# Performance work log

Hardware: AMD Instinct MI355X
Metric: run time of the kernel (lower is better)

## Reference

```python
import jax, jax.numpy as jnp
import numpy as np

B, N, C, H = 64, 198, 768, 12
D = C // H  # head_dim = 64


def lsq_binary(x, alpha):
    """Elastic (LSQ-style) symmetric binarization with STE: out = alpha*sign(x/alpha)."""
    xs = x / alpha
    return alpha * (xs + jax.lax.stop_gradient(jnp.sign(xs) - xs))


def lsq_bin01(x, alpha):
    """Asymmetric binarization to levels {0, alpha} with STE (for post-softmax attention)."""
    xs = x / alpha
    qh = jnp.clip(jnp.round(xs), 0.0, 1.0)
    return alpha * (xs + jax.lax.stop_gradient(qh - xs))


def gsb(x, alphas, bin_fn):
    """Group-superposition binarization: sum of residual binarizations with per-group scales."""
    out = jnp.zeros_like(x)
    r = x
    for a in alphas:  # fixed small loop over 3 groups
        b = bin_fn(r, a)
        out = out + b
        r = r - b
    return out


def bwn(w):
    """Binary-weight-network weight fake-quant (layerwise scale = mean|w|) with STE."""
    q = jnp.mean(jnp.abs(w)) * jnp.sign(w)
    return w + jax.lax.stop_gradient(q - w)


def setup_inputs() -> dict:
    key = jax.random.key(0)
    ks = jax.random.split(key, 8)
    one = jnp.ones((), jnp.float32)
    return {
        "x": jax.random.normal(ks[0], (B, N, C), jnp.float32),
        "qkv_w": jax.random.normal(ks[1], (3 * C, C), jnp.float32) * 0.02,
        "proj_w": jax.random.normal(ks[2], (C, C), jnp.float32) * 0.02,
        "proj_b": jnp.zeros((C,), jnp.float32),
        "move_q_b": jax.random.normal(ks[3], (H, 1, D), jnp.float32) * 0.01,
        "move_k_b": jax.random.normal(ks[4], (H, 1, D), jnp.float32) * 0.01,
        "move_v_b": jax.random.normal(ks[5], (H, 1, D), jnp.float32) * 0.01,
        "move_att_b": jax.random.normal(ks[6], (H, N, N), jnp.float32) * 0.01,
        "clip_in_qkv": one, "clip_query": one, "clip_key": one,
        "clip_v1": one, "clip_v2": one * 0.5, "clip_v3": one * 0.25,
        "clip_a1": one, "clip_a2": one * 0.5, "clip_a3": one * 0.25,
        "clip_in_proj": one,
    }


def reference(x, qkv_w, proj_w, proj_b, move_q_b, move_k_b, move_v_b, move_att_b,
              clip_in_qkv, clip_query, clip_key, clip_v1, clip_v2, clip_v3,
              clip_a1, clip_a2, clip_a3, clip_in_proj):
    b, n, c = x.shape
    scale = D ** -0.5
    # quantized qkv projection (binary act, BWN weight)
    xq = lsq_binary(x, clip_in_qkv)
    qkv = jnp.einsum('bnc,oc->bno', xq, bwn(qkv_w))  # [B,N,3C]
    qkv = qkv.reshape(b, n, 3, H, D).transpose(2, 0, 3, 1, 4)  # [3,B,H,N,D]
    q, k, v = qkv[0], qkv[1], qkv[2]
    # learnable per-head bias shifts, then fake-quant
    q = lsq_binary(q + move_q_b, clip_query)
    k = lsq_binary(k + move_k_b, clip_key)
    v = gsb(v + move_v_b, (clip_v1, clip_v2, clip_v3), lsq_binary)
    attn = jax.nn.softmax(jnp.einsum('bhnd,bhmd->bhnm', q, k) * scale, axis=-1)
    attn = attn + move_att_b  # [H,N,N] broadcast over batch
    attn = gsb(attn, (clip_a1, clip_a2, clip_a3), lsq_bin01)
    out = jnp.einsum('bhnm,bhmd->bhnd', attn, v).transpose(0, 2, 1, 3).reshape(b, n, c)
    # quantized output projection
    outq = lsq_binary(out, clip_in_proj)
    return jnp.einsum('bnc,oc->bno', outq, bwn(proj_w)) + proj_b
```

## Files before the change

kernel.cpp:

```cpp
#include <hip/hip_runtime.h>
#include <hip/hip_bf16.h>

typedef __attribute__((ext_vector_type(8))) short short8;
typedef __attribute__((ext_vector_type(4))) float f32x4;
typedef __attribute__((ext_vector_type(4))) int int4v;
typedef __attribute__((ext_vector_type(8))) char char8v;
typedef __attribute__((ext_vector_type(4), aligned(4))) unsigned int uint4a;

static constexpr int B = 64, N = 198, C = 768, H = 12, D = 64;
static constexpr int M = B * N;
static constexpr int BH = B * H;
static constexpr int O3C = 3 * C;
static constexpr int NXB = 99;
static constexpr int TLD8 = 144;
static constexpr int AL8 = 272;
static constexpr int VNP = 256;

static constexpr size_t OFF_MEANS = 0;
static constexpr size_t OFF_TAB   = 256;
static constexpr size_t OFF_PARTA = 2048;
static constexpr size_t OFF_PARTP = 4096;
static constexpr size_t OFF_XS    = 8192;
static constexpr size_t SZ_XS     = (size_t)M * C;
static constexpr size_t OFF_WQS   = OFF_XS + SZ_XS;
static constexpr size_t SZ_WQS    = (size_t)O3C * C;
static constexpr size_t OFF_WPS   = OFF_WQS + SZ_WQS;
static constexpr size_t SZ_WPS    = (size_t)C * C;
static constexpr size_t OFF_Q     = OFF_WPS + SZ_WPS;
static constexpr size_t SZ_QK8    = (size_t)BH * N * D;
static constexpr size_t OFF_K     = OFF_Q + SZ_QK8;
static constexpr size_t OFF_VT    = OFF_K + SZ_QK8;
static constexpr size_t SZ_VT8    = (size_t)BH * D * VNP;
static constexpr size_t OFF_OS    = OFF_VT + SZ_VT8;

#define GLOAD_LDS16(g, l)                                                  \
  __builtin_amdgcn_global_load_lds(                                        \
      (const __attribute__((address_space(1))) void*)(g),                  \
      (__attribute__((address_space(3))) void*)(l), 16, 0, 0)

__global__ void reduce_abs2_kernel(const float* __restrict__ qw, int nq,
                                   const float* __restrict__ pw, int np,
                                   double* __restrict__ partA, double* __restrict__ partP) {
  __shared__ double sm[256];
  const float* src;
  int n, b;
  double* dst;
  if (blockIdx.x < 256) { src = qw; n = nq; dst = partA; b = blockIdx.x; }
  else                  { src = pw; n = np; dst = partP; b = blockIdx.x - 256; }
  double s = 0.0;
  for (int i = b * 256 + threadIdx.x; i < n; i += 256 * 256)
    s += (double)fabsf(src[i]);
  sm[threadIdx.x] = s;
  __syncthreads();
  for (int off = 128; off > 0; off >>= 1) {
    if (threadIdx.x < (unsigned)off) sm[threadIdx.x] += sm[threadIdx.x + off];
    __syncthreads();
  }
  if (threadIdx.x == 0) dst[b] = sm[0];
}

__global__ void finalize_kernel(const double* __restrict__ pA, const double* __restrict__ pP,
                                double* __restrict__ means, double* __restrict__ tab,
                                const float* cq, const float* ck) {
  __shared__ double sm[256];
  int t = threadIdx.x;
  sm[t] = pA[t];
  __syncthreads();
  for (int off = 128; off > 0; off >>= 1) { if (t < off) sm[t] += sm[t + off]; __syncthreads(); }
  if (t == 0) means[0] = sm[0] / (double)((size_t)O3C * C);
  __syncthreads();
  sm[t] = pP[t];
  __syncthreads();
  for (int off = 128; off > 0; off >>= 1) { if (t < off) sm[t] += sm[t + off]; __syncthreads(); }
  if (t == 0) means[1] = sm[0] / (double)((size_t)C * C);
  double delta = (double)cq[0] * (double)ck[0] * 0.125;
  if (t < 129) tab[t] = exp((double)(t - 128) * delta);
  if (t < 16) tab[129 + t] = exp((double)t * delta);
}

__global__ void sign8_all_kernel(const float* __restrict__ x, signed char* __restrict__ Xs,
                                 const float* __restrict__ qw, signed char* __restrict__ Wq,
                                 const float* __restrict__ pw, signed char* __restrict__ Wp,
                                 int nx8, int nq8, int np8, const float* alpha) {
  float a = alpha[0];
  signed char posx = (a > 0.0f) ? 1 : ((a < 0.0f) ? -1 : 0);
  int total = nx8 + nq8 + np8;
  int stride = 256 * gridDim.x;
  for (int i = blockIdx.x * 256 + threadIdx.x; i < total; i += stride) {
    const float* src;
    signed char* dst;
    int j;
    signed char pos;
    if (i < nx8) { src = x; dst = Xs; j = i; pos = posx; }
    else if (i < nx8 + nq8) { src = qw; dst = Wq; j = i - nx8; pos = 1; }
    else { src = pw; dst = Wp; j = i - nx8 - nq8; pos = 1; }
    signed char neg = (signed char)(-pos);
    const float4* xp = (const float4*)(src + (size_t)j * 8);
    float4 u = xp[0], v = xp[1];
    float vals[8] = {u.x, u.y, u.z, u.w, v.x, v.y, v.z, v.w};
    char8v s;
#pragma unroll
    for (int k = 0; k < 8; ++k)
      s[k] = vals[k] > 0.0f ? pos : (vals[k] < 0.0f ? neg : (signed char)0);
    *(char8v*)(dst + (size_t)j * 8) = s;
  }
}

static __device__ inline bool xcd_decode(int lin, int nyb, int& x, int& y) {
  int k = lin & 7;
  int q = lin >> 3;
  int xi = q / nyb;
  y = q - xi * nyb;
  x = xi * 8 + k;
  return x < NXB;
}

static __device__ inline void stage_i8(const signed char* __restrict__ A,
                                       const signed char* __restrict__ Bmat,
                                       int i0, int o0, int k0,
                                       char* AsB, char* BsB) {
  int tid = threadIdx.x;
  int lane = tid & 63, w = tid >> 6;
#pragma unroll
  for (int c = 0; c < 2; ++c) {
    int ccb = w * 64 + c * 256;
    int cc = ccb + lane;
    int row = cc >> 2, cwl = cc & 3;
    int sc16 = (cwl ^ ((row >> 1) & 3)) * 16;
    GLOAD_LDS16(&A[(size_t)(i0 + row) * C + k0 + sc16], AsB + (size_t)ccb * 16);
    GLOAD_LDS16(&Bmat[(size_t)(o0 + row) * C + k0 + sc16], BsB + (size_t)ccb * 16);
  }
}

static __device__ inline void compute_i8(const signed char (*As)[64],
                                         const signed char (*Bs)[64],
                                         int4v acc[4][4]) {
  int lane = threadIdx.x & 63, w = threadIdx.x >> 6, wr = w >> 1, wc = w & 1;
  int g = lane >> 4;
  int4v af[4], bf[4];
#pragma unroll
  for (int m = 0; m < 4; ++m) {
    int row = wr * 64 + m * 16 + (lane & 15);
    af[m] = *(const int4v*)&As[row][((g ^ ((row >> 1) & 3))) * 16];
  }
#pragma unroll
  for (int n2 = 0; n2 < 4; ++n2) {
    int row = wc * 64 + n2 * 16 + (lane & 15);
    bf[n2] = *(const int4v*)&Bs[row][((g ^ ((row >> 1) & 3))) * 16];
  }
  __builtin_amdgcn_s_setprio(1);
#pragma unroll
  for (int m = 0; m < 4; ++m)
#pragma unroll
    for (int n2 = 0; n2 < 4; ++n2)
      acc[m][n2] = __builtin_amdgcn_mfma_i32_16x16x64_i8(af[m], bf[n2], acc[m][n2], 0, 0, 0);
  __builtin_amdgcn_s_setprio(0);
}

static __device__ inline void gemm_dbuf_i8(const signed char* __restrict__ A,
                                           const signed char* __restrict__ Bmat,
                                           int i0, int o0, char* smem, int4v acc[4][4]) {
  stage_i8(A, Bmat, i0, o0, 0, smem, smem + 8192);
  asm volatile("s_waitcnt vmcnt(0)" ::: "memory");
  __builtin_amdgcn_sched_barrier(0);
  __builtin_amdgcn_s_barrier();
#pragma unroll
  for (int t = 0; t < 12; ++t) {
    const int cu = t & 1;
    if (t < 11)
      stage_i8(A, Bmat, i0, o0, (t + 1) * 64,
               smem + (cu ^ 1) * 16384, smem + (cu ^ 1) * 16384 + 8192);
    compute_i8((const signed char(*)[64])(smem + cu * 16384),
               (const signed char(*)[64])(smem + cu * 16384 + 8192), acc);
    if (t < 11) {
      asm volatile("s_waitcnt vmcnt(0)" ::: "memory");
      __builtin_amdgcn_sched_barrier(0);
      __builtin_amdgcn_s_barrier();
    }
  }
}

__global__ __launch_bounds__(256) void gemm1_kernel(
    const signed char* __restrict__ Xs, const signed char* __restrict__ Wqs,
    const double* __restrict__ means,
    const float* cin, const float* cq, const float* ck,
    const float* cv1, const float* cv2, const float* cv3,
    const float* __restrict__ movq, const float* __restrict__ movk, const float* __restrict__ movv,
    signed char* __restrict__ Qs8, signed char* __restrict__ Ks8, signed char* __restrict__ Vt8) {
  int bx, by;
  if (!xcd_decode(blockIdx.x, O3C / 128, bx, by)) return;
  __shared__ __align__(16) char smem[32768];
  signed char* tile8 = (signed char*)smem;
  int4v acc[4][4] = {};
  int i0 = bx * 128, o0 = by * 128;
  gemm_dbuf_i8(Xs, Wqs, i0, o0, smem, acc);
  int tid = threadIdx.x;
  int lane = tid & 63, w = tid >> 6, wr = w >> 1, wc = w & 1;
  double cw_ = (double)cin[0] * means[0];
  float dq = cq[0], dk = ck[0];
  signed char sq8 = dq > 0.0f ? 1 : (dq < 0.0f ? -1 : 0);
  signed char sk8 = dk > 0.0f ? 1 : (dk < 0.0f ? -1 : 0);
  double aa1 = fabs((double)cv1[0]), aa2 = fabs((double)cv2[0]), aa3 = fabs((double)cv3[0]);
  int t = o0 / C;
  int rem0 = o0 - t * C;
  signed char sg8 = t == 0 ? sq8 : sk8;
  const float* mov = t == 0 ? movq : (t == 1 ? movk : movv);
  __syncthreads();
#pragma unroll
  for (int m = 0; m < 4; ++m)
#pragma unroll
    for (int n2 = 0; n2 < 4; ++n2)
#pragma unroll
      for (int r = 0; r < 4; ++r) {
        int rowL = wr * 64 + m * 16 + (lane >> 4) * 4 + r;
        int colL = wc * 64 + n2 * 16 + (lane & 15);
        int rem = rem0 + colL;
        int h = rem >> 6, d = rem & 63;
        double g = (double)acc[m][n2][r] * cw_;
        if (t < 2) {
          double v = g + (double)mov[h * D + d];
          tile8[rowL * TLD8 + colL] = v > 0.0 ? sg8 : (v < 0.0 ? (signed char)(-sg8) : (signed char)0);
        } else {
          double rr = g + (double)mov[h * D + d];
          double b1 = rr > 0.0 ? aa1 : (rr < 0.0 ? -aa1 : 0.0);
          rr -= b1;
          double b2 = rr > 0.0 ? aa2 : (rr < 0.0 ? -aa2 : 0.0);
          rr -= b2;
          double b3 = rr > 0.0 ? aa3 : (rr < 0.0 ? -aa3 : 0.0);
          tile8[colL * TLD8 + rowL] = (signed char)(int)rint(4.0 * (b1 + b2 + b3));
        }
      }
  __syncthreads();
  if (t < 2) {
    signed char* dst = t == 0 ? Qs8 : Ks8;
#pragma unroll
    for (int it = 0; it < 4; ++it) {
      int c = tid + it * 256;
      int rowL = c >> 3, cch = c & 7;
      int gr = i0 + rowL;
      int b = gr / N, nn = gr - b * N;
      int rem = rem0 + cch * 16;
      int h = rem >> 6, d = rem & 63;
      *(uint4a*)&dst[((size_t)(b * H + h) * N + nn) * 64 + d] =
          *(const uint4a*)&tile8[rowL * TLD8 + cch * 16];
    }
  } else {
#pragma unroll
    for (int it = 0; it < 4; ++it) {
      int c = tid + it * 256;
      int colL = c >> 3, tch = c & 7;
      int rem = rem0 + colL;
      int h = rem >> 6, d = rem & 63;
      int gr0 = i0 + tch * 16;
      int b0 = gr0 / N, nn0 = gr0 - b0 * N;
      if (nn0 + 16 <= N) {
        *(uint4a*)&Vt8[((size_t)(b0 * H + h) * 64 + d) * VNP + nn0] =
            *(const uint4a*)&tile8[colL * TLD8 + tch * 16];
      } else {
#pragma unroll
        for (int j = 0; j < 16; ++j) {
          int gr = gr0 + j;
          int b = gr / N, nn = gr - b * N;
          Vt8[((size_t)(b * H + h) * 64 + d) * VNP + nn] = tile8[colL * TLD8 + tch * 16 + j];
        }
      }
    }
  }
}

__global__ __launch_bounds__(256) void attn_kernel(
    const signed char* __restrict__ Qs8, const signed char* __restrict__ Ks8,
    const signed char* __restrict__ Vt8, const double* __restrict__ tab,
    const float* __restrict__ movatt,
    const float* ca1p, const float* ca2p, const float* ca3p, const float* cipp,
    signed char* __restrict__ Os) {
  __shared__ double Tl1[9];
  __shared__ double Tl2[16];
  __shared__ signed char Al8[4][16 * AL8];
  int i = blockIdx.x;
  int xcd = i & 7;
  int q = i >> 3;
  int rt = q % 13;
  int grp = q / 13;
  int tid = threadIdx.x;
  int w = tid >> 6, lane = tid & 63;
  int bh = (grp * 4 + w) * 8 + xcd;
  int b = bh / H, h = bh - b * H;
  int g = lane >> 4, q16 = lane & 15;
  if (tid < 9) Tl1[tid] = tab[16 * tid];
  if (tid >= 32 && tid < 48) Tl2[tid - 32] = tab[129 + (tid - 32)];
  for (int ii = lane; ii < 192; ii += 64) {
    int row = ii / 12, cd = ii - row * 12;
    *(int*)&Al8[w][row * AL8 + 208 + cd * 4] = 0;
  }
  __syncthreads();
  double ca1 = (double)ca1p[0], ca2 = (double)ca2p[0], ca3 = (double)ca3p[0];
  double t1 = 0.5 * ca1, t2 = 0.5 * ca2, t3 = 0.5 * ca3;
  int q1 = (int)rint(4.0 * ca1), q2 = (int)rint(4.0 * ca2), q3 = (int)rint(4.0 * ca3);
  float cip = cipp[0];
  signed char cp = cip > 0.0f ? 1 : (cip < 0.0f ? -1 : 0);

  int4v qf = {};
  int qrow = rt * 16 + q16;
  if (qrow < N) qf = *(const int4v*)&Qs8[((size_t)bh * N + qrow) * 64 + g * 16];
  int4v sacc[13] = {};
#pragma unroll
  for (int ct = 0; ct < 13; ++ct) {
    int krow = ct * 16 + q16;
    int4v kf = {};
    if (krow < N) kf = *(const int4v*)&Ks8[((size_t)bh * N + krow) * 64 + g * 16];
    sacc[ct] = __builtin_amdgcn_mfma_i32_16x16x64_i8(qf, kf, sacc[ct], 0, 0, 0);
  }
#pragma unroll
  for (int r = 0; r < 4; ++r) {
    int rowg = rt * 16 + g * 4 + r;
    int rowc = rowg < N ? rowg : N - 1;
    const float* mrow = movatt + ((size_t)h * N + rowc) * N;
    int mx = -1000000;
#pragma unroll
    for (int ct = 0; ct < 13; ++ct) {
      int colc = ct * 16 + q16;
      if (colc < N) mx = max(mx, sacc[ct][r]);
    }
    mx = max(mx, __shfl_xor(mx, 1));
    mx = max(mx, __shfl_xor(mx, 2));
    mx = max(mx, __shfl_xor(mx, 4));
    mx = max(mx, __shfl_xor(mx, 8));
    double ev[13];
    double ssum = 0.0;
#pragma unroll
    for (int ct = 0; ct < 13; ++ct) {
      int colc = ct * 16 + q16;
      int idx = sacc[ct][r] - mx + 128;
      idx = idx > 128 ? 128 : idx;
      double e = (colc < N) ? Tl1[idx >> 4] * Tl2[idx & 15] : 0.0;
      ev[ct] = e;
      ssum += e;
    }
    ssum += __shfl_xor(ssum, 1);
    ssum += __shfl_xor(ssum, 2);
    ssum += __shfl_xor(ssum, 4);
    ssum += __shfl_xor(ssum, 8);
    double rec = 1.0 / ssum;
#pragma unroll
    for (int ct = 0; ct < 13; ++ct) {
      int colc = ct * 16 + q16;
      int colb = colc < N ? colc : N - 1;
      double at = ev[ct] * rec + (double)mrow[colb];
      int p4 = 0;
      double rr = at;
      if (rr > t1) { p4 += q1; rr -= ca1; }
      if (rr > t2) { p4 += q2; rr -= ca2; }
      if (rr > t3) { p4 += q3; }
      Al8[w][(g * 4 + r) * AL8 + colc] = (signed char)((colc < N) ? p4 : 0);
    }
  }
  int4v oacc[4] = {};
#pragma unroll
  for (int kt = 0; kt < 4; ++kt) {
    int4v af = *(const int4v*)&Al8[w][q16 * AL8 + kt * 64 + g * 16];
#pragma unroll
    for (int dt = 0; dt < 4; ++dt) {
      int4v bv = *(const int4v*)&Vt8[((size_t)bh * 64 + dt * 16 + q16) * VNP + kt * 64 + g * 16];
      oacc[dt] = __builtin_amdgcn_mfma_i32_16x16x64_i8(af, bv, oacc[dt], 0, 0, 0);
    }
  }
#pragma unroll
  for (int dt = 0; dt < 4; ++dt)
#pragma unroll
    for (int r = 0; r < 4; ++r) {
      int rowg = rt * 16 + g * 4 + r;
      if (rowg < N) {
        int d = dt * 16 + q16;
        int s = oacc[dt][r];
        Os[((size_t)(b * N + rowg)) * C + h * D + d] =
            s > 0 ? cp : (s < 0 ? (signed char)(-cp) : (signed char)0);
      }
    }
}

__global__ __launch_bounds__(256) void gemm2_kernel(
    const signed char* __restrict__ Os, const signed char* __restrict__ Wps,
    const double* __restrict__ means, const float* cip, const float* __restrict__ proj_b,
    float* __restrict__ out) {
  int bx, by;
  if (!xcd_decode(blockIdx.x, C / 128, bx, by)) return;
  __shared__ __align__(16) char smem[32768];
  int4v acc[4][4] = {};
  int i0 = bx * 128, o0 = by * 128;
  gemm_dbuf_i8(Os, Wps, i0, o0, smem, acc);
  int lane = threadIdx.x & 63, w = threadIdx.x >> 6, wr = w >> 1, wc = w & 1;
  double cw_ = (double)cip[0] * means[1];
#pragma unroll
  for (int m = 0; m < 4; ++m)
#pragma unroll
    for (int n2 = 0; n2 < 4; ++n2)
#pragma unroll
      for (int r = 0; r < 4; ++r) {
        int row = i0 + wr * 64 + m * 16 + (lane >> 4) * 4 + r;
        int col = o0 + wc * 64 + n2 * 16 + (lane & 15);
        double v = (double)acc[m][n2][r] * cw_ + (double)proj_b[col];
        out[(size_t)row * C + col] = (float)v;
      }
}

extern "C" void kernel_launch(void* const* d_in, const int* in_sizes, int n_in,
                              void* d_out, int out_size, void* d_ws, size_t ws_size,
                              hipStream_t stream) {
  const float* x      = (const float*)d_in[0];
  const float* qkv_w  = (const float*)d_in[1];
  const float* proj_w = (const float*)d_in[2];
  const float* proj_b = (const float*)d_in[3];
  const float* movq   = (const float*)d_in[4];
  const float* movk   = (const float*)d_in[5];
  const float* movv   = (const float*)d_in[6];
  const float* movatt = (const float*)d_in[7];
  const float* c_inq  = (const float*)d_in[8];
  const float* c_q    = (const float*)d_in[9];
  const float* c_k    = (const float*)d_in[10];
  const float* c_v1   = (const float*)d_in[11];
  const float* c_v2   = (const float*)d_in[12];
  const float* c_v3   = (const float*)d_in[13];
  const float* c_a1   = (const float*)d_in[14];
  const float* c_a2   = (const float*)d_in[15];
  const float* c_a3   = (const float*)d_in[16];
  const float* c_inp  = (const float*)d_in[17];

  char* ws = (char*)d_ws;
  double* means = (double*)(ws + OFF_MEANS);
  double* tab   = (double*)(ws + OFF_TAB);
  double* partA = (double*)(ws + OFF_PARTA);
  double* partP = (double*)(ws + OFF_PARTP);
  signed char* Xs  = (signed char*)(ws + OFF_XS);
  signed char* Wqs = (signed char*)(ws + OFF_WQS);
  signed char* Wps = (signed char*)(ws + OFF_WPS);
  signed char* Qs8 = (signed char*)(ws + OFF_Q);
  signed char* Ks8 = (signed char*)(ws + OFF_K);
  signed char* Vt8 = (signed char*)(ws + OFF_VT);
  signed char* Os  = (signed char*)(ws + OFF_OS);

  reduce_abs2_kernel<<<512, 256, 0, stream>>>(qkv_w, O3C * C, proj_w, C * C, partA, partP);
  finalize_kernel<<<1, 256, 0, stream>>>(partA, partP, means, tab, c_q, c_k);
  sign8_all_kernel<<<2048, 256, 0, stream>>>(x, Xs, qkv_w, Wqs, proj_w, Wps,
                                             M * C / 8, O3C * C / 8, C * C / 8, c_inq);
  gemm1_kernel<<<104 * (O3C / 128), 256, 0, stream>>>(
      Xs, Wqs, means, c_inq, c_q, c_k, c_v1, c_v2, c_v3, movq, movk, movv, Qs8, Ks8, Vt8);
  attn_kernel<<<8 * 13 * (BH / 32), 256, 0, stream>>>(Qs8, Ks8, Vt8, tab, movatt, c_a1, c_a2, c_a3, c_inp, Os);
  gemm2_kernel<<<104 * (C / 128), 256, 0, stream>>>(
      Os, Wps, means, c_inp, proj_b, (float*)d_out);
}
```

Before: 161.4 us.

## Pre-tile int8 operands into MFMA fragment layout and load GEMM fragments directly from global

The sign kernel now writes X, qkv weights and proj weights in a 16-row x 64-byte fragment-tiled layout. The attention kernel writes its output in the same layout, so each MFMA operand becomes one contiguous 16-byte-per-lane load. Both GEMMs drop the LDS double-buffered staging and barriers and read fragments straight from global memory into registers. Tiles change to 64x256, with each wave owning 64 output columns. This removes LDS traffic and sync overhead, but loses LDS reuse across waves and has no explicit prefetch, so global load latency may be exposed.

```diff
diff --git a/kernel.cpp b/kernel.cpp
--- a/kernel.cpp
+++ b/kernel.cpp
@@ -11,10 +11,14 @@
 static constexpr int M = B * N;
 static constexpr int BH = B * H;
 static constexpr int O3C = 3 * C;
-static constexpr int NXB = 99;
-static constexpr int TLD8 = 144;
+static constexpr int KC = 48;
+static constexpr int NXT = 198;
+static constexpr int NXTP = 200;
 static constexpr int AL8 = 272;
 static constexpr int VNP = 256;
+static constexpr int TLQ = 272;
+static constexpr int TLV = 80;
+
 
 static constexpr size_t OFF_MEANS = 0;
 static constexpr size_t OFF_TAB   = 256;
@@ -33,11 +37,6 @@
 static constexpr size_t SZ_VT8    = (size_t)BH * D * VNP;
 static constexpr size_t OFF_OS    = OFF_VT + SZ_VT8;
 
-#define GLOAD_LDS16(g, l)                                                  \
-  __builtin_amdgcn_global_load_lds(                                        \
-      (const __attribute__((address_space(1))) void*)(g),                  \
-      (__attribute__((address_space(3))) void*)(l), 16, 0, 0)
-
 __global__ void reduce_abs2_kernel(const float* __restrict__ qw, int nq,
                                    const float* __restrict__ pw, int np,
                                    double* __restrict__ partA, double* __restrict__ partP) {
@@ -78,105 +77,66 @@
   if (t < 16) tab[129 + t] = exp((double)t * delta);
 }
 
-__global__ void sign8_all_kernel(const float* __restrict__ x, signed char* __restrict__ Xs,
-                                 const float* __restrict__ qw, signed char* __restrict__ Wq,
-                                 const float* __restrict__ pw, signed char* __restrict__ Wp,
-                                 int nx8, int nq8, int np8, const float* alpha) {
+__global__ void sign8_tiled_kernel(const float* __restrict__ x, signed char* __restrict__ Xs,
+                                   const float* __restrict__ qw, signed char* __restrict__ Wq,
+                                   const float* __restrict__ pw, signed char* __restrict__ Wp,
+                                   int ux, int uq, int up, const float* alpha) {
   float a = alpha[0];
   signed char posx = (a > 0.0f) ? 1 : ((a < 0.0f) ? -1 : 0);
-  int total = nx8 + nq8 + np8;
+  int total = ux + uq + up;
   int stride = 256 * gridDim.x;
-  for (int i = blockIdx.x * 256 + threadIdx.x; i < total; i += stride) {
+  for (int u = blockIdx.x * 256 + threadIdx.x; u < total; u += stride) {
     const float* src;
     signed char* dst;
     int j;
     signed char pos;
-    if (i < nx8) { src = x; dst = Xs; j = i; pos = posx; }
-    else if (i < nx8 + nq8) { src = qw; dst = Wq; j = i - nx8; pos = 1; }
-    else { src = pw; dst = Wp; j = i - nx8 - nq8; pos = 1; }
+    if (u < ux) { src = x; dst = Xs; j = u; pos = posx; }
+    else if (u < ux + uq) { src = qw; dst = Wq; j = u - ux; pos = 1; }
+    else { src = pw; dst = Wp; j = u - ux - uq; pos = 1; }
     signed char neg = (signed char)(-pos);
-    const float4* xp = (const float4*)(src + (size_t)j * 8);
-    float4 u = xp[0], v = xp[1];
-    float vals[8] = {u.x, u.y, u.z, u.w, v.x, v.y, v.z, v.w};
-    char8v s;
-#pragma unroll
-    for (int k = 0; k < 8; ++k)
-      s[k] = vals[k] > 0.0f ? pos : (vals[k] < 0.0f ? neg : (signed char)0);
-    *(char8v*)(dst + (size_t)j * 8) = s;
-  }
-}
-
-static __device__ inline bool xcd_decode(int lin, int nyb, int& x, int& y) {
+    int row = j / KC, kc = j - row * KC;
+    const float4* xp = (const float4*)(src + (size_t)row * C + kc * 16);
+    signed char out16[16];
+#pragma unroll
+    for (int q4 = 0; q4 < 4; ++q4) {
+      float4 v = xp[q4];
+      float vv[4] = {v.x, v.y, v.z, v.w};
+#pragma unroll
+      for (int k = 0; k < 4; ++k)
+        out16[q4 * 4 + k] = vv[k] > 0.0f ? pos : (vv[k] < 0.0f ? neg : (signed char)0);
+    }
+    size_t off = (((size_t)(row >> 4) * KC + kc) * 16 + (row & 15)) * 16;
+    *(uint4a*)(dst + off) = *(const uint4a*)out16;
+  }
+}
+
+static __device__ inline bool xcd_decode(int lin, int nyb, int limit, int& x, int& y) {
   int k = lin & 7;
   int q = lin >> 3;
   int xi = q / nyb;
   y = q - xi * nyb;
   x = xi * 8 + k;
-  return x < NXB;
-}
-
-static __device__ inline void stage_i8(const signed char* __restrict__ A,
-                                       const signed char* __restrict__ Bmat,
-                                       int i0, int o0, int k0,
-                                       char* AsB, char* BsB) {
-  int tid = threadIdx.x;
-  int lane = tid & 63, w = tid >> 6;
-#pragma unroll
-  for (int c = 0; c < 2; ++c) {
-    int ccb = w * 64 + c * 256;
-    int cc = ccb + lane;
-    int row = cc >> 2, cwl = cc & 3;
-    int sc16 = (cwl ^ ((row >> 1) & 3)) * 16;
-    GLOAD_LDS16(&A[(size_t)(i0 + row) * C + k0 + sc16], AsB + (size_t)ccb * 16);
-    GLOAD_LDS16(&Bmat[(size_t)(o0 + row) * C + k0 + sc16], BsB + (size_t)ccb * 16);
-  }
-}
-
-static __device__ inline void compute_i8(const signed char (*As)[64],
-                                         const signed char (*Bs)[64],
-                                         int4v acc[4][4]) {
-  int lane = threadIdx.x & 63, w = threadIdx.x >> 6, wr = w >> 1, wc = w & 1;
-  int g = lane >> 4;
-  int4v af[4], bf[4];
-#pragma unroll
-  for (int m = 0; m < 4; ++m) {
-    int row = wr * 64 + m * 16 + (lane & 15);
-    af[m] = *(const int4v*)&As[row][((g ^ ((row >> 1) & 3))) * 16];
-  }
-#pragma unroll
-  for (int n2 = 0; n2 < 4; ++n2) {
-    int row = wc * 64 + n2 * 16 + (lane & 15);
-    bf[n2] = *(const int4v*)&Bs[row][((g ^ ((row >> 1) & 3))) * 16];
-  }
-  __builtin_amdgcn_s_setprio(1);
-#pragma unroll
-  for (int m = 0; m < 4; ++m)
+  return x < limit;
+}
+
+static __device__ inline void gemm_reg_i8(const signed char* __restrict__ At,
+                                          const signed char* __restrict__ Bt,
+                                          int x4, int nt0, int4v acc[4][4]) {
+  int lane = threadIdx.x & 63;
+#pragma unroll
+  for (int t = 0; t < 12; ++t) {
+    int4v af[4], bf[4];
+#pragma unroll
+    for (int m = 0; m < 4; ++m)
+      af[m] = *(const int4v*)&At[((size_t)(x4 + m) * KC + t * 4) * 256 + lane * 16];
 #pragma unroll
     for (int n2 = 0; n2 < 4; ++n2)
-      acc[m][n2] = __builtin_amdgcn_mfma_i32_16x16x64_i8(af[m], bf[n2], acc[m][n2], 0, 0, 0);
-  __builtin_amdgcn_s_setprio(0);
-}
-
-static __device__ inline void gemm_dbuf_i8(const signed char* __restrict__ A,
-                                           const signed char* __restrict__ Bmat,
-                                           int i0, int o0, char* smem, int4v acc[4][4]) {
-  stage_i8(A, Bmat, i0, o0, 0, smem, smem + 8192);
-  asm volatile("s_waitcnt vmcnt(0)" ::: "memory");
-  __builtin_amdgcn_sched_barrier(0);
-  __builtin_amdgcn_s_barrier();
-#pragma unroll
-  for (int t = 0; t < 12; ++t) {
-    const int cu = t & 1;
-    if (t < 11)
-      stage_i8(A, Bmat, i0, o0, (t + 1) * 64,
-               smem + (cu ^ 1) * 16384, smem + (cu ^ 1) * 16384 + 8192);
-    compute_i8((const signed char(*)[64])(smem + cu * 16384),
-               (const signed char(*)[64])(smem + cu * 16384 + 8192), acc);
-    if (t < 11) {
-      asm volatile("s_waitcnt vmcnt(0)" ::: "memory");
-      __builtin_amdgcn_sched_barrier(0);
-      __builtin_amdgcn_s_barrier();
-    }
+      bf[n2] = *(const int4v*)&Bt[((size_t)(nt0 + n2) * KC + t * 4) * 256 + lane * 16];
+#pragma unroll
+    for (int m = 0; m < 4; ++m)
+#pragma unroll
+      for (int n2 = 0; n2 < 4; ++n2)
+        acc[m][n2] = __builtin_amdgcn_mfma_i32_16x16x64_i8(af[m], bf[n2], acc[m][n2], 0, 0, 0);
   }
 }
 
@@ -188,46 +148,44 @@
     const float* __restrict__ movq, const float* __restrict__ movk, const float* __restrict__ movv,
     signed char* __restrict__ Qs8, signed char* __restrict__ Ks8, signed char* __restrict__ Vt8) {
   int bx, by;
-  if (!xcd_decode(blockIdx.x, O3C / 128, bx, by)) return;
-  __shared__ __align__(16) char smem[32768];
-  signed char* tile8 = (signed char*)smem;
+  if (!xcd_decode(blockIdx.x, 9, NXT, bx, by)) return;
+  __shared__ __align__(16) signed char tile8[20480];
+  int tid = threadIdx.x;
+  int lane = tid & 63, w = tid >> 6;
   int4v acc[4][4] = {};
-  int i0 = bx * 128, o0 = by * 128;
-  gemm_dbuf_i8(Xs, Wqs, i0, o0, smem, acc);
-  int tid = threadIdx.x;
-  int lane = tid & 63, w = tid >> 6, wr = w >> 1, wc = w & 1;
+  gemm_reg_i8(Xs, Wqs, bx * 4, by * 16 + w * 4, acc);
   double cw_ = (double)cin[0] * means[0];
   float dq = cq[0], dk = ck[0];
   signed char sq8 = dq > 0.0f ? 1 : (dq < 0.0f ? -1 : 0);
   signed char sk8 = dk > 0.0f ? 1 : (dk < 0.0f ? -1 : 0);
   double aa1 = fabs((double)cv1[0]), aa2 = fabs((double)cv2[0]), aa3 = fabs((double)cv3[0]);
-  int t = o0 / C;
-  int rem0 = o0 - t * C;
+  int t = by / 3;
+  int rem0 = (by - t * 3) * 256;
   signed char sg8 = t == 0 ? sq8 : sk8;
   const float* mov = t == 0 ? movq : (t == 1 ? movk : movv);
-  __syncthreads();
+  int g = lane >> 4, q16 = lane & 15;
 #pragma unroll
   for (int m = 0; m < 4; ++m)
 #pragma unroll
     for (int n2 = 0; n2 < 4; ++n2)
 #pragma unroll
       for (int r = 0; r < 4; ++r) {
-        int rowL = wr * 64 + m * 16 + (lane >> 4) * 4 + r;
-        int colL = wc * 64 + n2 * 16 + (lane & 15);
+        int rowL = m * 16 + g * 4 + r;
+        int colL = w * 64 + n2 * 16 + q16;
         int rem = rem0 + colL;
         int h = rem >> 6, d = rem & 63;
-        double g = (double)acc[m][n2][r] * cw_;
+        double gg = (double)acc[m][n2][r] * cw_;
         if (t < 2) {
-          double v = g + (double)mov[h * D + d];
-          tile8[rowL * TLD8 + colL] = v > 0.0 ? sg8 : (v < 0.0 ? (signed char)(-sg8) : (signed char)0);
+          double v = gg + (double)mov[h * D + d];
+          tile8[rowL * TLQ + colL] = v > 0.0 ? sg8 : (v < 0.0 ? (signed char)(-sg8) : (signed char)0);
         } else {
-          double rr = g + (double)mov[h * D + d];
+          double rr = gg + (double)mov[h * D + d];
           double b1 = rr > 0.0 ? aa1 : (rr < 0.0 ? -aa1 : 0.0);
           rr -= b1;
           double b2 = rr > 0.0 ? aa2 : (rr < 0.0 ? -aa2 : 0.0);
           rr -= b2;
           double b3 = rr > 0.0 ? aa3 : (rr < 0.0 ? -aa3 : 0.0);
-          tile8[colL * TLD8 + rowL] = (signed char)(int)rint(4.0 * (b1 + b2 + b3));
+          tile8[colL * TLV + rowL] = (signed char)(int)rint(4.0 * (b1 + b2 + b3));
         }
       }
   __syncthreads();
@@ -236,32 +194,32 @@
 #pragma unroll
     for (int it = 0; it < 4; ++it) {
       int c = tid + it * 256;
-      int rowL = c >> 3, cch = c & 7;
-      int gr = i0 + rowL;
+      int rowL = c >> 4, cch = c & 15;
+      int gr = bx * 64 + rowL;
       int b = gr / N, nn = gr - b * N;
       int rem = rem0 + cch * 16;
       int h = rem >> 6, d = rem & 63;
       *(uint4a*)&dst[((size_t)(b * H + h) * N + nn) * 64 + d] =
-          *(const uint4a*)&tile8[rowL * TLD8 + cch * 16];
+          *(const uint4a*)&tile8[rowL * TLQ + cch * 16];
     }
   } else {
 #pragma unroll
     for (int it = 0; it < 4; ++it) {
       int c = tid + it * 256;
-      int colL = c >> 3, tch = c & 7;
+      int colL = c >> 2, tch = c & 3;
       int rem = rem0 + colL;
       int h = rem >> 6, d = rem & 63;
-      int gr0 = i0 + tch * 16;
+      int gr0 = bx * 64 + tch * 16;
       int b0 = gr0 / N, nn0 = gr0 - b0 * N;
       if (nn0 + 16 <= N) {
         *(uint4a*)&Vt8[((size_t)(b0 * H + h) * 64 + d) * VNP + nn0] =
-            *(const uint4a*)&tile8[colL * TLD8 + tch * 16];
+            *(const uint4a*)&tile8[colL * TLV + tch * 16];
       } else {
 #pragma unroll
         for (int j = 0; j < 16; ++j) {
           int gr = gr0 + j;
           int b = gr / N, nn = gr - b * N;
-          Vt8[((size_t)(b * H + h) * 64 + d) * VNP + nn] = tile8[colL * TLD8 + tch * 16 + j];
+          Vt8[((size_t)(b * H + h) * 64 + d) * VNP + nn] = tile8[colL * TLV + tch * 16 + j];
         }
       }
     }
@@ -371,34 +329,34 @@
     for (int r = 0; r < 4; ++r) {
       int rowg = rt * 16 + g * 4 + r;
       if (rowg < N) {
-        int d = dt * 16 + q16;
+        size_t grow = (size_t)b * N + rowg;
         int s = oacc[dt][r];
-        Os[((size_t)(b * N + rowg)) * C + h * D + d] =
+        Os[(grow >> 4) * (KC * 256) + (size_t)(h * 4 + dt) * 256 + (grow & 15) * 16 + q16] =
             s > 0 ? cp : (s < 0 ? (signed char)(-cp) : (signed char)0);
       }
     }
 }
 
 __global__ __launch_bounds__(256) void gemm2_kernel(
-    const signed char* __restrict__ Os, const signed char* __restrict__ Wps,
+    const signed char* __restrict__ Ot, const signed char* __restrict__ Wps,
     const double* __restrict__ means, const float* cip, const float* __restrict__ proj_b,
     float* __restrict__ out) {
   int bx, by;
-  if (!xcd_decode(blockIdx.x, C / 128, bx, by)) return;
-  __shared__ __align__(16) char smem[32768];
+  if (!xcd_decode(blockIdx.x, 3, NXT, bx, by)) return;
+  int tid = threadIdx.x;
+  int lane = tid & 63, w = tid >> 6;
   int4v acc[4][4] = {};
-  int i0 = bx * 128, o0 = by * 128;
-  gemm_dbuf_i8(Os, Wps, i0, o0, smem, acc);
-  int lane = threadIdx.x & 63, w = threadIdx.x >> 6, wr = w >> 1, wc = w & 1;
+  gemm_reg_i8(Ot, Wps, bx * 4, by * 16 + w * 4, acc);
   double cw_ = (double)cip[0] * means[1];
+  int g = lane >> 4, q16 = lane & 15;
 #pragma unroll
   for (int m = 0; m < 4; ++m)
 #pragma unroll
     for (int n2 = 0; n2 < 4; ++n2)
 #pragma unroll
       for (int r = 0; r < 4; ++r) {
-        int row = i0 + wr * 64 + m * 16 + (lane >> 4) * 4 + r;
-        int col = o0 + wc * 64 + n2 * 16 + (lane & 15);
+        int row = bx * 64 + m * 16 + g * 4 + r;
+        int col = by * 256 + w * 64 + n2 * 16 + q16;
         double v = (double)acc[m][n2][r] * cw_ + (double)proj_b[col];
         out[(size_t)row * C + col] = (float)v;
       }
@@ -441,11 +399,11 @@
 
   reduce_abs2_kernel<<<512, 256, 0, stream>>>(qkv_w, O3C * C, proj_w, C * C, partA, partP);
   finalize_kernel<<<1, 256, 0, stream>>>(partA, partP, means, tab, c_q, c_k);
-  sign8_all_kernel<<<2048, 256, 0, stream>>>(x, Xs, qkv_w, Wqs, proj_w, Wps,
-                                             M * C / 8, O3C * C / 8, C * C / 8, c_inq);
-  gemm1_kernel<<<104 * (O3C / 128), 256, 0, stream>>>(
+  sign8_tiled_kernel<<<2048, 256, 0, stream>>>(x, Xs, qkv_w, Wqs, proj_w, Wps,
+                                               M * KC, O3C * KC, C * KC, c_inq);
+  gemm1_kernel<<<NXTP * 9, 256, 0, stream>>>(
       Xs, Wqs, means, c_inq, c_q, c_k, c_v1, c_v2, c_v3, movq, movk, movv, Qs8, Ks8, Vt8);
   attn_kernel<<<8 * 13 * (BH / 32), 256, 0, stream>>>(Qs8, Ks8, Vt8, tab, movatt, c_a1, c_a2, c_a3, c_inp, Os);
-  gemm2_kernel<<<104 * (C / 128), 256, 0, stream>>>(
+  gemm2_kernel<<<NXTP * 3, 256, 0, stream>>>(
       Os, Wps, means, c_inp, proj_b, (float*)d_out);
 }
```

After: 174.4 us. 8.1% more time.

## Single-buffer int8 GEMM LDS and split gemm1 epilogue into two halves

Applied to the files above, without the earlier changes.

Replaces the double-buffered LDS pipeline in both int8 GEMMs with a single 16 KB buffer that loads, waits, computes and barriers each K step. The gemm1 epilogue tile now holds half the output at a time, written in two passes, so it fits in the smaller LDS allocation. The aim is to halve LDS per block and allow more resident blocks per CU. The cost is losing the overlap of global loads with MFMA work and adding extra barriers.

```diff
diff --git a/kernel.cpp b/kernel.cpp
--- a/kernel.cpp
+++ b/kernel.cpp
@@ -12,7 +12,8 @@
 static constexpr int BH = B * H;
 static constexpr int O3C = 3 * C;
 static constexpr int NXB = 99;
-static constexpr int TLD8 = 144;
+static constexpr int NXBP = 104;
+static constexpr int TL = 144;
 static constexpr int AL8 = 272;
 static constexpr int VNP = 256;
 
@@ -157,26 +158,18 @@
   __builtin_amdgcn_s_setprio(0);
 }
 
-static __device__ inline void gemm_dbuf_i8(const signed char* __restrict__ A,
+static __device__ inline void gemm_sbuf_i8(const signed char* __restrict__ A,
                                            const signed char* __restrict__ Bmat,
                                            int i0, int o0, char* smem, int4v acc[4][4]) {
-  stage_i8(A, Bmat, i0, o0, 0, smem, smem + 8192);
-  asm volatile("s_waitcnt vmcnt(0)" ::: "memory");
-  __builtin_amdgcn_sched_barrier(0);
-  __builtin_amdgcn_s_barrier();
 #pragma unroll
   for (int t = 0; t < 12; ++t) {
-    const int cu = t & 1;
-    if (t < 11)
-      stage_i8(A, Bmat, i0, o0, (t + 1) * 64,
-               smem + (cu ^ 1) * 16384, smem + (cu ^ 1) * 16384 + 8192);
-    compute_i8((const signed char(*)[64])(smem + cu * 16384),
-               (const signed char(*)[64])(smem + cu * 16384 + 8192), acc);
-    if (t < 11) {
-      asm volatile("s_waitcnt vmcnt(0)" ::: "memory");
-      __builtin_amdgcn_sched_barrier(0);
-      __builtin_amdgcn_s_barrier();
-    }
+    stage_i8(A, Bmat, i0, o0, t * 64, smem, smem + 8192);
+    asm volatile("s_waitcnt vmcnt(0)" ::: "memory");
+    __builtin_amdgcn_sched_barrier(0);
+    __builtin_amdgcn_s_barrier();
+    compute_i8((const signed char(*)[64])smem,
+               (const signed char(*)[64])(smem + 8192), acc);
+    __builtin_amdgcn_s_barrier();
   }
 }
 
@@ -189,11 +182,11 @@
     signed char* __restrict__ Qs8, signed char* __restrict__ Ks8, signed char* __restrict__ Vt8) {
   int bx, by;
   if (!xcd_decode(blockIdx.x, O3C / 128, bx, by)) return;
-  __shared__ __align__(16) char smem[32768];
+  __shared__ __align__(16) char smem[16384];
   signed char* tile8 = (signed char*)smem;
   int4v acc[4][4] = {};
   int i0 = bx * 128, o0 = by * 128;
-  gemm_dbuf_i8(Xs, Wqs, i0, o0, smem, acc);
+  gemm_sbuf_i8(Xs, Wqs, i0, o0, smem, acc);
   int tid = threadIdx.x;
   int lane = tid & 63, w = tid >> 6, wr = w >> 1, wc = w & 1;
   double cw_ = (double)cin[0] * means[0];
@@ -205,65 +198,87 @@
   int rem0 = o0 - t * C;
   signed char sg8 = t == 0 ? sq8 : sk8;
   const float* mov = t == 0 ? movq : (t == 1 ? movk : movv);
-  __syncthreads();
-#pragma unroll
-  for (int m = 0; m < 4; ++m)
-#pragma unroll
-    for (int n2 = 0; n2 < 4; ++n2)
-#pragma unroll
-      for (int r = 0; r < 4; ++r) {
-        int rowL = wr * 64 + m * 16 + (lane >> 4) * 4 + r;
-        int colL = wc * 64 + n2 * 16 + (lane & 15);
-        int rem = rem0 + colL;
-        int h = rem >> 6, d = rem & 63;
-        double g = (double)acc[m][n2][r] * cw_;
-        if (t < 2) {
-          double v = g + (double)mov[h * D + d];
-          tile8[rowL * TLD8 + colL] = v > 0.0 ? sg8 : (v < 0.0 ? (signed char)(-sg8) : (signed char)0);
-        } else {
-          double rr = g + (double)mov[h * D + d];
-          double b1 = rr > 0.0 ? aa1 : (rr < 0.0 ? -aa1 : 0.0);
-          rr -= b1;
-          double b2 = rr > 0.0 ? aa2 : (rr < 0.0 ? -aa2 : 0.0);
-          rr -= b2;
-          double b3 = rr > 0.0 ? aa3 : (rr < 0.0 ? -aa3 : 0.0);
-          tile8[colL * TLD8 + rowL] = (signed char)(int)rint(4.0 * (b1 + b2 + b3));
-        }
-      }
+  int g = lane >> 4, q16 = lane & 15;
   __syncthreads();
   if (t < 2) {
     signed char* dst = t == 0 ? Qs8 : Ks8;
 #pragma unroll
-    for (int it = 0; it < 4; ++it) {
-      int c = tid + it * 256;
-      int rowL = c >> 3, cch = c & 7;
-      int gr = i0 + rowL;
-      int b = gr / N, nn = gr - b * N;
-      int rem = rem0 + cch * 16;
-      int h = rem >> 6, d = rem & 63;
-      *(uint4a*)&dst[((size_t)(b * H + h) * N + nn) * 64 + d] =
-          *(const uint4a*)&tile8[rowL * TLD8 + cch * 16];
+    for (int p = 0; p < 2; ++p) {
+      if (wr == p) {
+#pragma unroll
+        for (int m = 0; m < 4; ++m)
+#pragma unroll
+          for (int n2 = 0; n2 < 4; ++n2)
+#pragma unroll
+            for (int r = 0; r < 4; ++r) {
+              int rowLoc = m * 16 + g * 4 + r;
+              int colL = wc * 64 + n2 * 16 + q16;
+              int rem = rem0 + colL;
+              int h = rem >> 6, d = rem & 63;
+              double v = (double)acc[m][n2][r] * cw_ + (double)mov[h * D + d];
+              tile8[rowLoc * TL + colL] =
+                  v > 0.0 ? sg8 : (v < 0.0 ? (signed char)(-sg8) : (signed char)0);
+            }
+      }
+      __syncthreads();
+#pragma unroll
+      for (int it = 0; it < 2; ++it) {
+        int c = tid + it * 256;
+        int rowLoc = c >> 3, cch = c & 7;
+        int gr = i0 + p * 64 + rowLoc;
+        int b = gr / N, nn = gr - b * N;
+        int rem = rem0 + cch * 16;
+        int h = rem >> 6, d = rem & 63;
+        *(uint4a*)&dst[((size_t)(b * H + h) * N + nn) * 64 + d] =
+            *(const uint4a*)&tile8[rowLoc * TL + cch * 16];
+      }
+      __syncthreads();
     }
   } else {
 #pragma unroll
-    for (int it = 0; it < 4; ++it) {
-      int c = tid + it * 256;
-      int colL = c >> 3, tch = c & 7;
-      int rem = rem0 + colL;
-      int h = rem >> 6, d = rem & 63;
-      int gr0 = i0 + tch * 16;
-      int b0 = gr0 / N, nn0 = gr0 - b0 * N;
-      if (nn0 + 16 <= N) {
-        *(uint4a*)&Vt8[((size_t)(b0 * H + h) * 64 + d) * VNP + nn0] =
-            *(const uint4a*)&tile8[colL * TLD8 + tch * 16];
-      } else {
-#pragma unroll
-        for (int j = 0; j < 16; ++j) {
-          int gr = gr0 + j;
-          int b = gr / N, nn = gr - b * N;
-          Vt8[((size_t)(b * H + h) * 64 + d) * VNP + nn] = tile8[colL * TLD8 + tch * 16 + j];
+    for (int p = 0; p < 2; ++p) {
+      if (wc == p) {
+#pragma unroll
+        for (int m = 0; m < 4; ++m)
+#pragma unroll
+          for (int n2 = 0; n2 < 4; ++n2)
+#pragma unroll
+            for (int r = 0; r < 4; ++r) {
+              int rowL = wr * 64 + m * 16 + g * 4 + r;
+              int colLoc = n2 * 16 + q16;
+              int rem = rem0 + p * 64 + colLoc;
+              int h = rem >> 6, d = rem & 63;
+              double rr = (double)acc[m][n2][r] * cw_ + (double)mov[h * D + d];
+              double b1 = rr > 0.0 ? aa1 : (rr < 0.0 ? -aa1 : 0.0);
+              rr -= b1;
+              double b2 = rr > 0.0 ? aa2 : (rr < 0.0 ? -aa2 : 0.0);
+              rr -= b2;
+              double b3 = rr > 0.0 ? aa3 : (rr < 0.0 ? -aa3 : 0.0);
+              tile8[colLoc * TL + rowL] = (signed char)(int)rint(4.0 * (b1 + b2 + b3));
+            }
+      }
+      __syncthreads();
+#pragma unroll
+      for (int it = 0; it < 2; ++it) {
+        int c = tid + it * 256;
+        int colLoc = c >> 3, tch = c & 7;
+        int rem = rem0 + p * 64 + colLoc;
+        int h = rem >> 6, d = rem & 63;
+        int gr0 = i0 + tch * 16;
+        int b0 = gr0 / N, nn0 = gr0 - b0 * N;
+        if (nn0 + 16 <= N) {
+          *(uint4a*)&Vt8[((size_t)(b0 * H + h) * 64 + d) * VNP + nn0] =
+              *(const uint4a*)&tile8[colLoc * TL + tch * 16];
+        } else {
+#pragma unroll
+          for (int j = 0; j < 16; ++j) {
+            int gr = gr0 + j;
+            int b = gr / N, nn = gr - b * N;
+            Vt8[((size_t)(b * H + h) * 64 + d) * VNP + nn] = tile8[colLoc * TL + tch * 16 + j];
+          }
         }
       }
+      __syncthreads();
     }
   }
 }
@@ -385,10 +400,10 @@
     float* __restrict__ out) {
   int bx, by;
   if (!xcd_decode(blockIdx.x, C / 128, bx, by)) return;
-  __shared__ __align__(16) char smem[32768];
+  __shared__ __align__(16) char smem[16384];
   int4v acc[4][4] = {};
   int i0 = bx * 128, o0 = by * 128;
-  gemm_dbuf_i8(Os, Wps, i0, o0, smem, acc);
+  gemm_sbuf_i8(Os, Wps, i0, o0, smem, acc);
   int lane = threadIdx.x & 63, w = threadIdx.x >> 6, wr = w >> 1, wc = w & 1;
   double cw_ = (double)cip[0] * means[1];
 #pragma unroll
@@ -443,9 +458,9 @@
   finalize_kernel<<<1, 256, 0, stream>>>(partA, partP, means, tab, c_q, c_k);
   sign8_all_kernel<<<2048, 256, 0, stream>>>(x, Xs, qkv_w, Wqs, proj_w, Wps,
                                              M * C / 8, O3C * C / 8, C * C / 8, c_inq);
-  gemm1_kernel<<<104 * (O3C / 128), 256, 0, stream>>>(
+  gemm1_kernel<<<NXBP * (O3C / 128), 256, 0, stream>>>(
       Xs, Wqs, means, c_inq, c_q, c_k, c_v1, c_v2, c_v3, movq, movk, movv, Qs8, Ks8, Vt8);
   attn_kernel<<<8 * 13 * (BH / 32), 256, 0, stream>>>(Qs8, Ks8, Vt8, tab, movatt, c_a1, c_a2, c_a3, c_inp, Os);
-  gemm2_kernel<<<104 * (C / 128), 256, 0, stream>>>(
+  gemm2_kernel<<<NXBP * (C / 128), 256, 0, stream>>>(
       Os, Wps, means, c_inp, proj_b, (float*)d_out);
 }
```

Result: slower. 166.2 us (+3.0%).
